# Performance work log

Hardware: AMD Instinct MI355X
Metric: run time of the kernel (lower is better)

Reference implementation:

```python
import jax, jax.numpy as jnp
import numpy as np

B, S, E, H, V, T, L = 64, 512, 512, 512, 32000, 2, 1


def setup_inputs() -> dict:
    key = jax.random.key(0)
    ks = jax.random.split(key, 12)
    # xavier_normal std for h0/c0 of shape (L, B, H): fan_in=B*H, fan_out=L*H
    xav = float(np.sqrt(2.0 / (B * H + L * H)))
    s = 1.0 / float(np.sqrt(H))  # pytorch LSTM default uniform bound
    return {
        "sentence": jax.random.randint(ks[0], (B, S), 0, V, dtype=jnp.int64),
        "h0": jax.random.normal(ks[1], (L, B, H), jnp.float32) * xav,
        "c0": jax.random.normal(ks[2], (L, B, H), jnp.float32) * xav,
        "emb": jax.random.normal(ks[3], (V, E), jnp.float32),
        "W_ih": jax.random.uniform(ks[4], (4 * H, E), jnp.float32, -s, s),
        "W_hh": jax.random.uniform(ks[5], (4 * H, H), jnp.float32, -s, s),
        "b_ih": jax.random.uniform(ks[6], (4 * H,), jnp.float32, -s, s),
        "b_hh": jax.random.uniform(ks[7], (4 * H,), jnp.float32, -s, s),
        "W_lin": jax.random.uniform(ks[8], (T, H), jnp.float32, -s, s),
        "b_lin": jax.random.uniform(ks[9], (T,), jnp.float32, -s, s),
    }


def reference(sentence, h0, c0, emb, W_ih, W_hh, b_ih, b_hh, W_lin, b_lin):
    x = emb[sentence]                                   # [B,S,E]
    # precompute input-to-gate projections for all timesteps
    xg = jnp.einsum("bse,ge->bsg", x, W_ih) + (b_ih + b_hh)  # [B,S,4H]

    def step(carry, xt):
        h, c = carry                                    # [B,H] each
        g = xt + h @ W_hh.T                             # [B,4H]
        i, f, gc, o = jnp.split(g, 4, axis=-1)          # torch gate order i,f,g,o
        i = jax.nn.sigmoid(i)
        f = jax.nn.sigmoid(f)
        gc = jnp.tanh(gc)
        o = jax.nn.sigmoid(o)
        c = f * c + i * gc
        h = o * jnp.tanh(c)
        return (h, c), h

    (hn, cn), hs = jax.lax.scan(step, (h0[0], c0[0]), xg.transpose(1, 0, 2))
    lstm_out = hs.transpose(1, 0, 2)                    # [B,S,H]
    # dropout is identity at inference; torch code indexes drop[-1,:,:] =
    # LAST BATCH SAMPLE (batch_first=True quirk) -> [S,H]
    last = lstm_out[-1]                                 # [S,H]
    return last @ W_lin.T + b_lin                       # [S,T]
```

## Files before the change

kernel.cpp:

```cpp
#include <hip/hip_runtime.h>
#include <hip/hip_bf16.h>


#define NB 64

#define HIDX(e) ((((e) >> 4) * 20) + ((e) & 15))

__global__ __launch_bounds__(256) void xg_gemm_k(
    const int* __restrict__ sent, const float* __restrict__ emb,
    const float* __restrict__ W_ih, const float* __restrict__ b_ih,
    const float* __restrict__ b_hh, float* __restrict__ xg)
{
    __shared__ float As[16][65];
    __shared__ float Bs[16][65];
    __shared__ int aidx[64];
    const int tid = threadIdx.x;
    const int t0 = blockIdx.x * 64;
    const int n0 = blockIdx.y * 64;
    if (tid < 64) aidx[tid] = sent[63 * 512 + t0 + tid];
    __syncthreads();

    const int kk = tid & 15;
    const int mm = tid >> 4;
    const int tx = tid & 15, ty = tid >> 4;
    float acc[4][4] = {};

    for (int kb = 0; kb < 512; kb += 16) {
        #pragma unroll
        for (int j = 0; j < 4; j++) {
            int m = mm + j * 16;
            As[kk][m] = emb[(size_t)aidx[m] * 512 + kb + kk];
            Bs[kk][m] = W_ih[(size_t)(n0 + m) * 512 + kb + kk];
        }
        __syncthreads();
        #pragma unroll
        for (int k = 0; k < 16; k++) {
            float a[4], bv[4];
            #pragma unroll
            for (int i = 0; i < 4; i++) a[i] = As[k][ty * 4 + i];
            #pragma unroll
            for (int j = 0; j < 4; j++) bv[j] = Bs[k][tx * 4 + j];
            #pragma unroll
            for (int i = 0; i < 4; i++)
                #pragma unroll
                for (int j = 0; j < 4; j++)
                    acc[i][j] += a[i] * bv[j];
        }
        __syncthreads();
    }

    #pragma unroll
    for (int i = 0; i < 4; i++) {
        int t = t0 + ty * 4 + i;
        #pragma unroll
        for (int j = 0; j < 4; j++) {
            int col = n0 + tx * 4 + j;
            int q = col >> 9, bb = (col >> 3) & 63, jj = col & 7;
            xg[(size_t)t * 2048 + bb * 32 + q * 8 + jj] =
                acc[i][j] + b_ih[col] + b_hh[col];
        }
    }
}

__global__ __launch_bounds__(256, 1) void lstm_seq_k(
    const float* __restrict__ h0, const float* __restrict__ c0,
    const float* __restrict__ W_hh, const float* __restrict__ xg,
    float* __restrict__ hs,
    unsigned long long* __restrict__ sA,
    unsigned long long* __restrict__ sB)
{
    __shared__ float lw[32 * 512];
    __shared__ float hbuf[32 * 20];

    const int tid = threadIdx.x;
    const int b = blockIdx.x;
    const int cg = tid & 31;
    const int rg = tid >> 5;
    const int hidx = b * 8 + rg;

    {
        const int lr  = tid >> 3;
        const int seg = tid & 7;
        const int q   = lr >> 3;
        const int jj  = lr & 7;
        const float* src = &W_hh[(size_t)(q * 512 + b * 8 + jj) * 512 + seg * 64];
        #pragma unroll
        for (int f = 0; f < 16; f++) {
            float4 v = *(const float4*)&src[f * 4];
            int c0i = seg * 64 + f * 4;
            float vv[4] = {v.x, v.y, v.z, v.w};
            #pragma unroll
            for (int e4 = 0; e4 < 4; e4++) {
                int c = c0i + e4;
                lw[(lr * 8 + ((c & 15) >> 1)) * 64 + (c >> 4) * 2 + (c & 1)] = vv[e4];
            }
        }
    }

    float creg = c0[63 * 512 + hidx];
    __syncthreads();

    for (int t = 0; t < 512; t++) {
        float xgp[4];
        #pragma unroll
        for (int q = 0; q < 4; q++)
            xgp[q] = xg[(size_t)t * 2048 + b * 32 + q * 8 + rg];

        if (t == 0) {
            hbuf[HIDX(tid)]       = h0[63 * 512 + tid];
            hbuf[HIDX(tid + 256)] = h0[63 * 512 + tid + 256];
        } else {
            unsigned long long* src = ((t - 1) & 1) ? sB : sA;
            const unsigned int expt = (unsigned int)t;
            unsigned long long v0, v1;
            for (;;) {
                v0 = __hip_atomic_load(&src[tid],       __ATOMIC_RELAXED, __HIP_MEMORY_SCOPE_AGENT);
                v1 = __hip_atomic_load(&src[tid + 256], __ATOMIC_RELAXED, __HIP_MEMORY_SCOPE_AGENT);
                if ((unsigned int)(v0 >> 32) == expt &&
                    (unsigned int)(v1 >> 32) == expt) break;
            }
            hbuf[HIDX(tid)]       = __uint_as_float((unsigned int)v0);
            hbuf[HIDX(tid + 256)] = __uint_as_float((unsigned int)v1);
        }
        __syncthreads();

        float hvf[16];
        #pragma unroll
        for (int i4 = 0; i4 < 4; i4++) {
            float4 v = *(const float4*)&hbuf[cg * 20 + i4 * 4];
            hvf[i4 * 4 + 0] = v.x; hvf[i4 * 4 + 1] = v.y;
            hvf[i4 * 4 + 2] = v.z; hvf[i4 * 4 + 3] = v.w;
        }

        float acc[4];
        #pragma unroll
        for (int q = 0; q < 4; q++) {
            const float* wrow = &lw[((q * 8 + rg) * 8) * 64 + cg * 2];
            float s = 0.f;
            #pragma unroll
            for (int kp = 0; kp < 8; kp++) {
                float2 wv = *(const float2*)&wrow[kp * 64];
                s += wv.x * hvf[kp * 2 + 0];
                s += wv.y * hvf[kp * 2 + 1];
            }
            acc[q] = s;
        }

        #pragma unroll
        for (int q = 0; q < 4; q++) {
            #pragma unroll
            for (int m = 16; m >= 1; m >>= 1)
                acc[q] += __shfl_xor(acc[q], m, 64);
        }

        float gi = acc[0] + xgp[0];
        float gf = acc[1] + xgp[1];
        float gg = acc[2] + xgp[2];
        float go = acc[3] + xgp[3];
        float ii = 1.f / (1.f + __expf(-gi));
        float ff = 1.f / (1.f + __expf(-gf));
        float cc = 1.f - 2.f / (__expf(2.f * gg) + 1.f);
        float oo = 1.f / (1.f + __expf(-go));
        creg = ff * creg + ii * cc;
        float th = 1.f - 2.f / (__expf(2.f * creg) + 1.f);
        float hval = oo * th;

        if (cg == 0) {
            hs[(size_t)t * 512 + hidx] = hval;
            unsigned long long* dst = (t & 1) ? sB : sA;
            unsigned long long pv =
                ((unsigned long long)(unsigned int)(t + 1) << 32) |
                (unsigned long long)__float_as_uint(hval);
            __hip_atomic_store(&dst[hidx], pv,
                               __ATOMIC_RELAXED, __HIP_MEMORY_SCOPE_AGENT);
        }
    }
}

__global__ __launch_bounds__(256) void final_linear_k(
    const float* __restrict__ hs, const float* __restrict__ W_lin,
    const float* __restrict__ b_lin, float* __restrict__ out)
{
    const int tid = threadIdx.x;
    const int wave = tid >> 6;
    const int lane = tid & 63;
    const int s = blockIdx.x * 4 + wave;
    const float* h = hs + (size_t)s * 512;
    float a0 = 0.f, a1 = 0.f;
    #pragma unroll
    for (int k0 = 0; k0 < 512; k0 += 64) {
        float hv = h[k0 + lane];
        a0 += hv * W_lin[k0 + lane];
        a1 += hv * W_lin[512 + k0 + lane];
    }
    #pragma unroll
    for (int m = 32; m >= 1; m >>= 1) {
        a0 += __shfl_xor(a0, m, 64);
        a1 += __shfl_xor(a1, m, 64);
    }
    if (lane == 0) {
        out[s * 2]     = a0 + b_lin[0];
        out[s * 2 + 1] = a1 + b_lin[1];
    }
}

extern "C" void kernel_launch(void* const* d_in, const int* in_sizes, int n_in,
                              void* d_out, int out_size, void* d_ws, size_t ws_size,
                              hipStream_t stream)
{
    const int*   sent  = (const int*)d_in[0];
    const float* h0    = (const float*)d_in[1];
    const float* c0    = (const float*)d_in[2];
    const float* emb   = (const float*)d_in[3];
    const float* W_ih  = (const float*)d_in[4];
    const float* W_hh  = (const float*)d_in[5];
    const float* b_ih  = (const float*)d_in[6];
    const float* b_hh  = (const float*)d_in[7];
    const float* W_lin = (const float*)d_in[8];
    const float* b_lin = (const float*)d_in[9];
    float* out = (float*)d_out;

    char* ws = (char*)d_ws;
    float* xg = (float*)ws;
    float* hs = (float*)(ws + 4 * 1024 * 1024);
    unsigned long long* sA = (unsigned long long*)(ws + 5 * 1024 * 1024);
    unsigned long long* sB = (unsigned long long*)(ws + 5 * 1024 * 1024 + 4096);

    hipMemsetAsync(sA, 0, 2 * 4096, stream);

    dim3 g1(8, 32);
    xg_gemm_k<<<g1, 256, 0, stream>>>(sent, emb, W_ih, b_ih, b_hh, xg);
    lstm_seq_k<<<NB, 256, 0, stream>>>(h0, c0, W_hh, xg, hs, sA, sB);
    final_linear_k<<<128, 256, 0, stream>>>(hs, W_lin, b_lin, out);
}
```

Baseline: 1.214 ms.

## Prefetch W_hh from LDS before the spin-wait and double-buffer the h buffer

Changes the LDS layout of W_hh so that each lane reads float4 chunks. Each step's 16 weight loads are issued into registers before the cross-block spin-wait, so their latency overlaps the barrier wait instead of following it. The h staging buffer is double-buffered by timestep parity so writes for the next step cannot race with reads from the previous one. An s_sleep is added inside the poll loop to ease contention on the atomic loads, at the risk of slightly later wakeups, and the held weights add register pressure.

```diff
diff --git a/kernel.cpp b/kernel.cpp
--- a/kernel.cpp
+++ b/kernel.cpp
@@ -70,7 +70,8 @@
     unsigned long long* __restrict__ sB)
 {
     __shared__ float lw[32 * 512];
-    __shared__ float hbuf[32 * 20];
+    __shared__ float hbufA[32 * 20];
+    __shared__ float hbufB[32 * 20];
 
     const int tid = threadIdx.x;
     const int b = blockIdx.x;
@@ -88,12 +89,9 @@
         for (int f = 0; f < 16; f++) {
             float4 v = *(const float4*)&src[f * 4];
             int c0i = seg * 64 + f * 4;
-            float vv[4] = {v.x, v.y, v.z, v.w};
-            #pragma unroll
-            for (int e4 = 0; e4 < 4; e4++) {
-                int c = c0i + e4;
-                lw[(lr * 8 + ((c & 15) >> 1)) * 64 + (c >> 4) * 2 + (c & 1)] = vv[e4];
-            }
+            int kq  = (c0i & 15) >> 2;
+            int cg4 = (c0i >> 4) * 4;
+            *(float4*)&lw[(size_t)(lr * 4 + kq) * 128 + cg4] = v;
         }
     }
 
@@ -101,14 +99,26 @@
     __syncthreads();
 
     for (int t = 0; t < 512; t++) {
+        float* hb = (t & 1) ? hbufB : hbufA;
+
+        float4 wv[4][4];
+        #pragma unroll
+        for (int q = 0; q < 4; q++) {
+            const float* wrow = &lw[(size_t)((q * 8 + rg) * 4) * 128 + cg * 4];
+            #pragma unroll
+            for (int kq = 0; kq < 4; kq++)
+                wv[q][kq] = *(const float4*)&wrow[kq * 128];
+        }
         float xgp[4];
         #pragma unroll
         for (int q = 0; q < 4; q++)
             xgp[q] = xg[(size_t)t * 2048 + b * 32 + q * 8 + rg];
 
+        asm volatile("" ::: "memory");
+
         if (t == 0) {
-            hbuf[HIDX(tid)]       = h0[63 * 512 + tid];
-            hbuf[HIDX(tid + 256)] = h0[63 * 512 + tid + 256];
+            hb[HIDX(tid)]       = h0[63 * 512 + tid];
+            hb[HIDX(tid + 256)] = h0[63 * 512 + tid + 256];
         } else {
             unsigned long long* src = ((t - 1) & 1) ? sB : sA;
             const unsigned int expt = (unsigned int)t;
@@ -118,16 +128,17 @@
                 v1 = __hip_atomic_load(&src[tid + 256], __ATOMIC_RELAXED, __HIP_MEMORY_SCOPE_AGENT);
                 if ((unsigned int)(v0 >> 32) == expt &&
                     (unsigned int)(v1 >> 32) == expt) break;
+                __builtin_amdgcn_s_sleep(1);
             }
-            hbuf[HIDX(tid)]       = __uint_as_float((unsigned int)v0);
-            hbuf[HIDX(tid + 256)] = __uint_as_float((unsigned int)v1);
+            hb[HIDX(tid)]       = __uint_as_float((unsigned int)v0);
+            hb[HIDX(tid + 256)] = __uint_as_float((unsigned int)v1);
         }
         __syncthreads();
 
         float hvf[16];
         #pragma unroll
         for (int i4 = 0; i4 < 4; i4++) {
-            float4 v = *(const float4*)&hbuf[cg * 20 + i4 * 4];
+            float4 v = *(const float4*)&hb[cg * 20 + i4 * 4];
             hvf[i4 * 4 + 0] = v.x; hvf[i4 * 4 + 1] = v.y;
             hvf[i4 * 4 + 2] = v.z; hvf[i4 * 4 + 3] = v.w;
         }
@@ -135,13 +146,13 @@
         float acc[4];
         #pragma unroll
         for (int q = 0; q < 4; q++) {
-            const float* wrow = &lw[((q * 8 + rg) * 8) * 64 + cg * 2];
             float s = 0.f;
             #pragma unroll
-            for (int kp = 0; kp < 8; kp++) {
-                float2 wv = *(const float2*)&wrow[kp * 64];
-                s += wv.x * hvf[kp * 2 + 0];
-                s += wv.y * hvf[kp * 2 + 1];
+            for (int kq = 0; kq < 4; kq++) {
+                s += wv[q][kq].x * hvf[kq * 4 + 0];
+                s += wv[q][kq].y * hvf[kq * 4 + 1];
+                s += wv[q][kq].z * hvf[kq * 4 + 2];
+                s += wv[q][kq].w * hvf[kq * 4 + 3];
             }
             acc[q] = s;
         }
```

Result: faster. 1.001 ms (-17.5%).
